# Kernel tuning notes

Measured on AMD Instinct MI355X. Metric: run time of the kernel, lower is better.

Reference implementation:

```python
import jax, jax.numpy as jnp
import numpy as np

D_MODEL = 512
D_STATE = 64
SEQ_LEN = 8192
BATCH = 8
LN_EPS = 1e-3  # keras LayerNormalization default epsilon
DELTA_MIN = 0.001
DELTA_MAX = 0.8 * (2.0 / D_STATE)  # default when use_hippo_init=True


def setup_inputs() -> dict:
    key = jax.random.key(0)
    ks = jax.random.split(key, 10)
    x = jax.random.normal(ks[0], (BATCH, SEQ_LEN, D_MODEL), dtype=jnp.float32)
    # Dense layers: glorot-uniform-ish init via scaled normal for simplicity
    def dense_w(k, fan_in, fan_out):
        lim = np.sqrt(6.0 / (fan_in + fan_out))
        return jax.random.uniform(k, (fan_in, fan_out), minval=-lim, maxval=lim, dtype=jnp.float32)
    W_in = dense_w(ks[1], D_MODEL, D_MODEL)
    b_in = jnp.zeros((D_MODEL,), jnp.float32)
    W_xs = dense_w(ks[2], D_MODEL, D_STATE)
    # HiPPO-LegS log init: A_log = log(n+1)
    A_log = jnp.log(jnp.arange(1, D_STATE + 1, dtype=jnp.float32))
    log_delta = jax.random.uniform(ks[3], (D_STATE,), minval=np.log(DELTA_MIN), maxval=np.log(DELTA_MAX), dtype=jnp.float32)
    B = jnp.ones((D_STATE,), jnp.float32)
    C = jax.random.normal(ks[4], (D_STATE,), dtype=jnp.float32)  # stddev=1.0
    D = jnp.ones((D_MODEL,), jnp.float32)
    W_so = dense_w(ks[5], D_STATE, D_MODEL)
    W_out = dense_w(ks[6], D_MODEL, D_MODEL)
    b_out = jnp.zeros((D_MODEL,), jnp.float32)
    ln_gamma = jnp.ones((D_MODEL,), jnp.float32)
    ln_beta = jnp.zeros((D_MODEL,), jnp.float32)
    return {
        "x": x, "ln_gamma": ln_gamma, "ln_beta": ln_beta,
        "W_in": W_in, "b_in": b_in, "W_xs": W_xs,
        "A_log": A_log, "log_delta": log_delta, "B": B, "C": C, "D": D,
        "W_so": W_so, "W_out": W_out, "b_out": b_out,
    }


def reference(x, ln_gamma, ln_beta, W_in, b_in, W_xs, A_log, log_delta, B, C, D, W_so, W_out, b_out):
    Bsz, L, dm = x.shape
    n_fft = 1 << int(np.ceil(np.log2(2 * L - 1)))
    residual = x
    # LayerNorm over last axis (keras default)
    mu = jnp.mean(x, axis=-1, keepdims=True)
    var = jnp.mean(jnp.square(x - mu), axis=-1, keepdims=True)
    xn = (x - mu) * jax.lax.rsqrt(var + LN_EPS) * ln_gamma + ln_beta
    z = xn @ W_in + b_in                       # (B, L, d_model)
    x_state = z @ W_xs                          # (B, L, d_state)
    # Diagonal SSM discretization (bilinear/Tustin)
    A = -jnp.exp(A_log)
    delta = jax.nn.softplus(log_delta)
    dA2 = delta * A / 2.0
    A_bar = (1.0 + dA2) / (1.0 - dA2)           # (d_state,)
    B_bar = delta / (1.0 - dA2) * B             # (d_state,)
    t = jnp.arange(L, dtype=jnp.float32)
    kernel = jnp.power(A_bar[None, :], t[:, None]) * B_bar[None, :]  # (L, d_state)
    # FFT convolution along time
    u_t = jnp.transpose(x_state, (0, 2, 1))     # (B, d_state, L)
    k_t = kernel.T                              # (d_state, L)
    u_f = jnp.fft.rfft(u_t, n=n_fft, axis=-1)
    k_f = jnp.fft.rfft(k_t, n=n_fft, axis=-1)
    y = jnp.fft.irfft(u_f * k_f[None, :, :], n=n_fft, axis=-1)[:, :, :L]
    y_state = jnp.transpose(y, (0, 2, 1))       # (B, L, d_state)
    y_state = y_state * C[None, None, :]
    y = y_state @ W_so                          # (B, L, d_model)
    y = y + D * z
    y = y @ W_out + b_out
    return y + residual
```

## Files before the change

### kernel.cpp

```cpp
#include <hip/hip_runtime.h>
#include <hip/hip_bf16.h>
#include <cstddef>
#include <cstdint>

#define DM 512
#define DS 64
#define L_SEQ 8192
#define NB 8
#define M_ROWS (NB * L_SEQ)
#define LN_EPS 1e-3f
#define NCHUNK 256
#define LCH 32

typedef __attribute__((ext_vector_type(8))) short short8;
typedef __attribute__((ext_vector_type(4))) float f32x4;
using bf16 = __hip_bfloat16;
using ushort_t = unsigned short;

__device__ __forceinline__ unsigned short f2bf(float f) {
    bf16 h = __float2bfloat16(f);
    return *reinterpret_cast<unsigned short*>(&h);
}

__device__ __forceinline__ int swzcol(int row, int col) {
    return (col & ~63) | (((((col >> 3) & 7) ^ (row & 7))) << 3) | (col & 7);
}

__device__ __forceinline__ size_t pkidx(int k, int n, int Kd32) {
    int n16 = n >> 4, fr = n & 15, kt = k >> 5, fq = (k >> 3) & 3, e = k & 7;
    return (((size_t)(n16 * Kd32 + kt) * 64 + fq * 16 + fr) << 3) + e;
}

__device__ __forceinline__ void gload_lds16(const void* g, void* l) {
    __builtin_amdgcn_global_load_lds(
        (const __attribute__((address_space(1))) void*)g,
        (__attribute__((address_space(3))) void*)l, 16, 0, 0);
}

template<int N> __device__ __forceinline__ void wait_vm() {
    static_assert(N == 0 || N == 2, "");
    if constexpr (N == 0) asm volatile("s_waitcnt vmcnt(0)" ::: "memory");
    else                  asm volatile("s_waitcnt vmcnt(2)" ::: "memory");
}

__device__ __forceinline__ void block_barrier() {
    asm volatile("" ::: "memory");
    __builtin_amdgcn_s_barrier();
    asm volatile("" ::: "memory");
}

__global__ __launch_bounds__(256) void prep(const float* __restrict__ W_so,
                                            const float* __restrict__ W_out,
                                            const float* __restrict__ W_in,
                                            const float* __restrict__ W_xs,
                                            const float* __restrict__ b_in,
                                            const float* __restrict__ b_out,
                                            const float* __restrict__ Dv,
                                            float* __restrict__ sWc2,
                                            float* __restrict__ sWc1,
                                            float* __restrict__ bc1,
                                            float* __restrict__ sWc3,
                                            float* __restrict__ bc2)
{
    int i = blockIdx.x * 256 + threadIdx.x;
    if (i < 32768) {
        int s = i >> 9, j = i & 511;
        float a = 0.f;
        for (int c = 0; c < 512; ++c) a += W_so[s * 512 + c] * W_out[c * 512 + j];
        sWc2[i] = a;
    } else if (i < 65536) {
        int idx = i - 32768; int k = idx >> 6, n = idx & 63;
        float a = 0.f;
        for (int c = 0; c < 512; ++c) a += W_in[k * 512 + c] * W_xs[c * 64 + n];
        sWc1[idx] = a;
    } else if (i < 65600) {
        int n = i - 65536;
        float a = 0.f;
        for (int c = 0; c < 512; ++c) a += b_in[c] * W_xs[c * 64 + n];
        bc1[n] = a;
    } else if (i < 327744) {
        int idx = i - 65600; int k = idx >> 9, j = idx & 511;
        float a = 0.f;
        for (int c = 0; c < 512; ++c) a += W_in[k * 512 + c] * Dv[c] * W_out[c * 512 + j];
        sWc3[idx] = a;
    } else if (i < 328256) {
        int j = i - 327744;
        float a = b_out[j];
        for (int c = 0; c < 512; ++c) a += b_in[c] * Dv[c] * W_out[c * 512 + j];
        bc2[j] = a;
    }
}

__global__ __launch_bounds__(256) void pack_all(const float* __restrict__ sWc3,
                                                const float* __restrict__ sWc1,
                                                const float* __restrict__ sWc2,
                                                ushort_t* __restrict__ Wc3Pk,
                                                ushort_t* __restrict__ Wc1Pk,
                                                ushort_t* __restrict__ Wc2Pk)
{
    int i = blockIdx.x * 256 + threadIdx.x;
    if (i < 262144) {
        int k = i >> 9, n = i & 511;
        Wc3Pk[pkidx(k, n, 16)] = f2bf(sWc3[i]);
    } else if (i < 294912) {
        int j = i - 262144; int k = j >> 6, n = j & 63;
        Wc1Pk[pkidx(k, n, 16)] = f2bf(sWc1[j]);
    } else if (i < 327680) {
        int j = i - 294912; int s = j >> 9, n = j & 511;
        Wc2Pk[pkidx(s, n, 2)] = f2bf(sWc2[j]);
    }
}

__global__ __launch_bounds__(64) void ln_kernel(const float* __restrict__ x,
                                                const float* __restrict__ gamma,
                                                const float* __restrict__ beta,
                                                ushort_t* __restrict__ xn)
{
    size_t row = blockIdx.x;
    int lane = threadIdx.x;
    const float4* xr = (const float4*)(x + row * DM);
    float4 v0 = xr[lane * 2];
    float4 v1 = xr[lane * 2 + 1];
    float s  = v0.x + v0.y + v0.z + v0.w + v1.x + v1.y + v1.z + v1.w;
    float s2 = v0.x*v0.x + v0.y*v0.y + v0.z*v0.z + v0.w*v0.w
             + v1.x*v1.x + v1.y*v1.y + v1.z*v1.z + v1.w*v1.w;
    #pragma unroll
    for (int off = 32; off > 0; off >>= 1) {
        s  += __shfl_xor(s,  off);
        s2 += __shfl_xor(s2, off);
    }
    float mu  = s * (1.0f / DM);
    float var = s2 * (1.0f / DM) - mu * mu;
    float rs  = rsqrtf(var + LN_EPS);
    const float4* g4 = (const float4*)gamma;
    const float4* b4 = (const float4*)beta;
    float4 g0 = g4[lane * 2], g1 = g4[lane * 2 + 1];
    float4 bb0 = b4[lane * 2], bb1 = b4[lane * 2 + 1];
    short8 o;
    o[0] = (short)f2bf((v0.x - mu) * rs * g0.x + bb0.x);
    o[1] = (short)f2bf((v0.y - mu) * rs * g0.y + bb0.y);
    o[2] = (short)f2bf((v0.z - mu) * rs * g0.z + bb0.z);
    o[3] = (short)f2bf((v0.w - mu) * rs * g0.w + bb0.w);
    o[4] = (short)f2bf((v1.x - mu) * rs * g1.x + bb1.x);
    o[5] = (short)f2bf((v1.y - mu) * rs * g1.y + bb1.y);
    o[6] = (short)f2bf((v1.z - mu) * rs * g1.z + bb1.z);
    o[7] = (short)f2bf((v1.w - mu) * rs * g1.w + bb1.w);
    int g = (lane & 7) ^ ((int)row & 7);
    *(short8*)(xn + row * DM + (lane >> 3) * 64 + g * 8) = o;
}

__device__ __forceinline__ void store_out(float* C, size_t i, float v) { C[i] = v; }
__device__ __forceinline__ void store_out(bf16* C, size_t i, float v)  { C[i] = __float2bfloat16(v); }

template<int BN, int WR, int WC, typename OutT, bool DUAL, bool HB, bool HA, bool SWZO>
__global__ __launch_bounds__(512, 4) void gemm_bp(const ushort_t* __restrict__ A1,
                                                  const ushort_t* __restrict__ B1,
                                                  const ushort_t* __restrict__ A2,
                                                  const ushort_t* __restrict__ B2,
                                                  const float* __restrict__ bias,
                                                  const float* __restrict__ aux,
                                                  OutT* __restrict__ C,
                                                  int M, int N, int K2)
{
    constexpr int BM = 128;
    constexpr int MF = BM / (16 * WR), NF = BN / (16 * WC);
    static_assert(NF == 2, "b ping-pong arrays assume NF==2");
    __shared__ unsigned char LDS[3][BM * 128];

    const int tid = threadIdx.x;
    const int lane = tid & 63, w = tid >> 6;
    const int fr = lane & 15, fq = lane >> 4;
    const int wr = w % WR, wc = w / WR;

    const int ny = N / BN;
    const int per = (int)gridDim.x >> 3;
    const int lg = ((int)blockIdx.x & 7) * per + ((int)blockIdx.x >> 3);
    const size_t bm0 = (size_t)(lg / ny) * BM;
    const int bn0 = (lg % ny) * BN;
    const int nk = (DUAL ? 1 : 0) + K2 / 64;

    f32x4 acc[MF][NF];
    #pragma unroll
    for (int m = 0; m < MF; ++m)
        #pragma unroll
        for (int n = 0; n < NF; ++n)
            acc[m][n] = (f32x4){0.f, 0.f, 0.f, 0.f};

    auto stage = [&](int buf, int t) {
        #pragma unroll
        for (int j = 0; j < 2; ++j) {
            int r = j * 64 + (tid >> 3);
            const ushort_t* src;
            if constexpr (DUAL) {
                if (t == 0) src = A1 + (bm0 + r) * (size_t)64 + (tid & 7) * 8;
                else        src = A2 + (bm0 + r) * (size_t)512 + (size_t)(t - 1) * 64 + (tid & 7) * 8;
            } else {
                src = A2 + (bm0 + r) * (size_t)K2 + (size_t)t * 64 + (tid & 7) * 8;
            }
            gload_lds16(src, &LDS[buf][j * 8192 + w * 1024]);
        }
    };

    auto loadB = [&](short8 (&bb)[2][2], int t) {
        #pragma unroll
        for (int h = 0; h < 2; ++h)
            #pragma unroll
            for (int n = 0; n < NF; ++n) {
                int n16g = (bn0 + wc * (BN / WC) + n * 16) >> 4;
                const ushort_t* p;
                if constexpr (DUAL) {
                    if (t == 0) p = B1 + (((size_t)(n16g * 2 + h) * 64 + lane) << 3);
                    else        p = B2 + (((size_t)(n16g * 16 + (t - 1) * 2 + h) * 64 + lane) << 3);
                } else {
                    p = B2 + (((size_t)(n16g * (K2 / 32) + t * 2 + h) * 64 + lane) << 3);
                }
                bb[h][n] = *(const short8*)p;
            }
    };

    auto compute = [&](int buf, const short8 (&bb)[2][2]) {
        #pragma unroll
        for (int h = 0; h < 2; ++h) {
            short8 af[MF];
            #pragma unroll
            for (int m = 0; m < MF; ++m) {
                int row = wr * (BM / WR) + m * 16 + fr;
                int g = (h * 4 + fq) ^ (row & 7);
                af[m] = *(const short8*)&LDS[buf][row * 128 + g * 16];
            }
            #pragma unroll
            for (int m = 0; m < MF; ++m)
                #pragma unroll
                for (int n = 0; n < NF; ++n)
                    acc[m][n] = __builtin_amdgcn_mfma_f32_16x16x32_bf16(af[m], bb[h][n], acc[m][n], 0, 0, 0);
        }
    };

    short8 bX[2][2], bY[2][2];
    stage(0, 0);
    loadB(bX, 0);
    if (nk > 1) stage(1, 1);

    #define PHASE(T, BCUR, BNEXT)                                            \
        do {                                                                 \
            if ((T) + 1 < nk) wait_vm<2>(); else wait_vm<0>();               \
            block_barrier();                                                 \
            if ((T) + 1 < nk) loadB(BNEXT, (T) + 1);                         \
            if ((T) + 2 < nk) stage(((T) + 2) % 3, (T) + 2);                 \
            __builtin_amdgcn_sched_barrier(0);                               \
            compute((T) % 3, BCUR);                                          \
        } while (0)

    for (int t = 0; t < nk; t += 2) {
        PHASE(t, bX, bY);
        if (t + 1 < nk) PHASE(t + 1, bY, bX);
    }
    #undef PHASE

    #pragma unroll
    for (int n = 0; n < NF; ++n) {
        int coll = wc * (BN / WC) + n * 16 + fr;
        int colg = bn0 + coll;
        float bv = HB ? bias[colg] : 0.f;
        #pragma unroll
        for (int m = 0; m < MF; ++m) {
            int rowl = wr * (BM / WR) + m * 16 + fq * 4;
            #pragma unroll
            for (int r = 0; r < 4; ++r) {
                size_t row = bm0 + rowl + r;
                float v = acc[m][n][r] + bv;
                if constexpr (HA) v += aux[row * (size_t)N + colg];
                size_t oc = SWZO ? (size_t)swzcol(rowl + r, colg) : (size_t)colg;
                store_out(C, row * (size_t)N + oc, v);
            }
        }
    }
}

__device__ __forceinline__ void ssm_params(const float* A_log, const float* log_delta,
                                           const float* Bv, int n, float& Ab, float& Bb)
{
    float A  = -expf(A_log[n]);
    float dl = log1pf(expf(log_delta[n]));
    float dA2 = dl * A * 0.5f;
    float inv = 1.0f / (1.0f - dA2);
    Ab = (1.0f + dA2) * inv;
    Bb = dl * inv * Bv[n];
}

__global__ __launch_bounds__(64) void scan_pass1(const float* __restrict__ xs,
                                                 const float* __restrict__ A_log,
                                                 const float* __restrict__ log_delta,
                                                 const float* __restrict__ Bv,
                                                 float* __restrict__ carry)
{
    int b = blockIdx.x / NCHUNK;
    int c = blockIdx.x % NCHUNK;
    int n = threadIdx.x;
    float Ab, Bb;
    ssm_params(A_log, log_delta, Bv, n, Ab, Bb);
    size_t base = ((size_t)b * L_SEQ + (size_t)c * LCH) * DS + n;
    float h = 0.0f;
    for (int t = 0; t < LCH; ++t)
        h = Ab * h + Bb * xs[base + (size_t)t * DS];
    carry[((size_t)b * NCHUNK + c) * DS + n] = h;
}

__global__ __launch_bounds__(64) void scan_pass2(const float* __restrict__ A_log,
                                                 const float* __restrict__ log_delta,
                                                 const float* __restrict__ Bv,
                                                 const float* __restrict__ carry,
                                                 float* __restrict__ hin)
{
    int b = blockIdx.x;
    int n = threadIdx.x;
    float Ab, Bb;
    ssm_params(A_log, log_delta, Bv, n, Ab, Bb);
    float powA = powf(Ab, (float)LCH);
    float h = 0.0f;
    for (int c = 0; c < NCHUNK; ++c) {
        size_t idx = ((size_t)b * NCHUNK + c) * DS + n;
        hin[idx] = h;
        h = powA * h + carry[idx];
    }
}

__global__ __launch_bounds__(64) void scan_pass3(const float* __restrict__ xs,
                                                 const float* __restrict__ A_log,
                                                 const float* __restrict__ log_delta,
                                                 const float* __restrict__ Bv,
                                                 const float* __restrict__ Cv,
                                                 const float* __restrict__ hin,
                                                 ushort_t* __restrict__ ys)
{
    int b = blockIdx.x / NCHUNK;
    int c = blockIdx.x % NCHUNK;
    int n = threadIdx.x;
    float Ab, Bb;
    ssm_params(A_log, log_delta, Bv, n, Ab, Bb);
    float Cn = Cv[n];
    size_t base = ((size_t)b * L_SEQ + (size_t)c * LCH) * DS + n;
    size_t rowbase = ((size_t)b * L_SEQ + (size_t)c * LCH) * DS;
    float h = hin[((size_t)b * NCHUNK + c) * DS + n];
    for (int t = 0; t < LCH; ++t) {
        h = Ab * h + Bb * xs[base + (size_t)t * DS];
        int col = (((n >> 3) ^ (t & 7)) << 3) | (n & 7);
        ys[rowbase + (size_t)t * DS + col] = f2bf(Cn * h);
    }
}

extern "C" void kernel_launch(void* const* d_in, const int* in_sizes, int n_in,
                              void* d_out, int out_size, void* d_ws, size_t ws_size,
                              hipStream_t stream)
{
    const float* x         = (const float*)d_in[0];
    const float* ln_gamma  = (const float*)d_in[1];
    const float* ln_beta   = (const float*)d_in[2];
    const float* W_in      = (const float*)d_in[3];
    const float* b_in      = (const float*)d_in[4];
    const float* W_xs      = (const float*)d_in[5];
    const float* A_log     = (const float*)d_in[6];
    const float* log_delta = (const float*)d_in[7];
    const float* Bv        = (const float*)d_in[8];
    const float* Cv        = (const float*)d_in[9];
    const float* Dv        = (const float*)d_in[10];
    const float* W_so      = (const float*)d_in[11];
    const float* W_out     = (const float*)d_in[12];
    const float* b_out     = (const float*)d_in[13];
    float* out = (float*)d_out;

    const size_t M = M_ROWS;
    float*    xs_f   = (float*)d_ws;
    ushort_t* xn_b   = (ushort_t*)(xs_f + M * DS);
    ushort_t* ys_b   = xn_b + M * (size_t)DM;
    ushort_t* Wc3Pk  = ys_b + M * (size_t)DS;
    ushort_t* Wc1Pk  = Wc3Pk + (size_t)DM * DM;
    ushort_t* Wc2Pk  = Wc1Pk + (size_t)DM * DS;
    float*    sWc2   = (float*)(Wc2Pk + (size_t)DS * DM);
    float*    sWc1   = sWc2 + (size_t)DS * DM;
    float*    bc1    = sWc1 + (size_t)DM * DS;
    float*    sWc3   = bc1 + 64;
    float*    bc2    = sWc3 + (size_t)DM * DM;
    float*    carry  = bc2 + DM;
    float*    hin    = carry + NB * NCHUNK * DS;

    prep<<<dim3(1283), dim3(256), 0, stream>>>(W_so, W_out, W_in, W_xs, b_in, b_out, Dv,
                                               sWc2, sWc1, bc1, sWc3, bc2);
    pack_all<<<dim3(1280), dim3(256), 0, stream>>>(sWc3, sWc1, sWc2, Wc3Pk, Wc1Pk, Wc2Pk);
    ln_kernel<<<dim3((unsigned)M), dim3(64), 0, stream>>>(x, ln_gamma, ln_beta, xn_b);
    gemm_bp<64, 4, 2, float, false, true, false, false>
        <<<dim3(M / 128), dim3(512), 0, stream>>>(nullptr, nullptr, xn_b, Wc1Pk,
                                                  bc1, nullptr, xs_f, (int)M, DS, DM);
    scan_pass1<<<dim3(NB * NCHUNK), dim3(64), 0, stream>>>(xs_f, A_log, log_delta, Bv, carry);
    scan_pass2<<<dim3(NB), dim3(64), 0, stream>>>(A_log, log_delta, Bv, carry, hin);
    scan_pass3<<<dim3(NB * NCHUNK), dim3(64), 0, stream>>>(xs_f, A_log, log_delta, Bv, Cv, hin, ys_b);
    gemm_bp<256, 1, 8, float, true, true, true, false>
        <<<dim3((M / 128) * (DM / 256)), dim3(512), 0, stream>>>(ys_b, Wc2Pk, xn_b, Wc3Pk,
                                                                 bc2, x, out, (int)M, DM, DM);
}
```

Measured before the change: 235.7 us.

## Make output GEMM persistent over multiple M tiles with overlapped epilogue and aux prefetch

The GEMM kernel now processes MT consecutive 128-row tiles per block, flattening tiles and K-steps into one pipelined stage sequence. The next tile's A loads stay in flight while the current tile's epilogue runs, and residual (aux) values are prefetched into registers before the last K-step of each tile. The final GEMM also moves from BN=256 (1x8 warps) to BN=128 (2x4 warps) with four M tiles per block, which cuts block count and launch/prologue overhead. The costs are more registers held for paux and hand-tuned vmcnt wait counts that must exactly match the number of outstanding loads.

```diff
diff --git a/kernel.cpp b/kernel.cpp
--- a/kernel.cpp
+++ b/kernel.cpp
@@ -38,9 +38,11 @@
 }
 
 template<int N> __device__ __forceinline__ void wait_vm() {
-    static_assert(N == 0 || N == 2, "");
-    if constexpr (N == 0) asm volatile("s_waitcnt vmcnt(0)" ::: "memory");
-    else                  asm volatile("s_waitcnt vmcnt(2)" ::: "memory");
+    static_assert(N == 0 || N == 2 || N == 18 || N == 34, "");
+    if constexpr (N == 0)       asm volatile("s_waitcnt vmcnt(0)" ::: "memory");
+    else if constexpr (N == 2)  asm volatile("s_waitcnt vmcnt(2)" ::: "memory");
+    else if constexpr (N == 18) asm volatile("s_waitcnt vmcnt(18)" ::: "memory");
+    else                        asm volatile("s_waitcnt vmcnt(34)" ::: "memory");
 }
 
 __device__ __forceinline__ void block_barrier() {
@@ -152,7 +154,8 @@
 __device__ __forceinline__ void store_out(float* C, size_t i, float v) { C[i] = v; }
 __device__ __forceinline__ void store_out(bf16* C, size_t i, float v)  { C[i] = __float2bfloat16(v); }
 
-template<int BN, int WR, int WC, typename OutT, bool DUAL, bool HB, bool HA, bool SWZO>
+template<int BN, int WR, int WC, int MT, int NKT, typename OutT,
+         bool DUAL, bool HB, bool HA, bool SWZO>
 __global__ __launch_bounds__(512, 4) void gemm_bp(const ushort_t* __restrict__ A1,
                                                   const ushort_t* __restrict__ B1,
                                                   const ushort_t* __restrict__ A2,
@@ -160,10 +163,12 @@
                                                   const float* __restrict__ bias,
                                                   const float* __restrict__ aux,
                                                   OutT* __restrict__ C,
-                                                  int M, int N, int K2)
+                                                  int M, int N)
 {
     constexpr int BM = 128;
     constexpr int MF = BM / (16 * WR), NF = BN / (16 * WC);
+    constexpr int NS = MT * NKT;
+    constexpr int WEPI = 2 + MF * NF * 4;
     static_assert(NF == 2, "b ping-pong arrays assume NF==2");
     __shared__ unsigned char LDS[3][BM * 128];
 
@@ -175,9 +180,8 @@
     const int ny = N / BN;
     const int per = (int)gridDim.x >> 3;
     const int lg = ((int)blockIdx.x & 7) * per + ((int)blockIdx.x >> 3);
-    const size_t bm0 = (size_t)(lg / ny) * BM;
+    const size_t bm0 = (size_t)(lg / ny) * (BM * MT);
     const int bn0 = (lg % ny) * BN;
-    const int nk = (DUAL ? 1 : 0) + K2 / 64;
 
     f32x4 acc[MF][NF];
     #pragma unroll
@@ -186,22 +190,27 @@
         for (int n = 0; n < NF; ++n)
             acc[m][n] = (f32x4){0.f, 0.f, 0.f, 0.f};
 
-    auto stage = [&](int buf, int t) {
+    float paux[MF][NF][4];
+
+    auto stage = [&](int buf, int s) {
+        int tt = s / NKT, kk = s % NKT;
+        size_t rb = bm0 + (size_t)tt * BM;
         #pragma unroll
         for (int j = 0; j < 2; ++j) {
             int r = j * 64 + (tid >> 3);
             const ushort_t* src;
             if constexpr (DUAL) {
-                if (t == 0) src = A1 + (bm0 + r) * (size_t)64 + (tid & 7) * 8;
-                else        src = A2 + (bm0 + r) * (size_t)512 + (size_t)(t - 1) * 64 + (tid & 7) * 8;
+                if (kk == 0) src = A1 + (rb + r) * (size_t)64 + (tid & 7) * 8;
+                else         src = A2 + (rb + r) * (size_t)512 + (size_t)(kk - 1) * 64 + (tid & 7) * 8;
             } else {
-                src = A2 + (bm0 + r) * (size_t)K2 + (size_t)t * 64 + (tid & 7) * 8;
+                src = A2 + (rb + r) * (size_t)512 + (size_t)kk * 64 + (tid & 7) * 8;
             }
             gload_lds16(src, &LDS[buf][j * 8192 + w * 1024]);
         }
     };
 
-    auto loadB = [&](short8 (&bb)[2][2], int t) {
+    auto loadB = [&](short8 (&bb)[2][2], int s) {
+        int kk = s % NKT;
         #pragma unroll
         for (int h = 0; h < 2; ++h)
             #pragma unroll
@@ -209,10 +218,10 @@
                 int n16g = (bn0 + wc * (BN / WC) + n * 16) >> 4;
                 const ushort_t* p;
                 if constexpr (DUAL) {
-                    if (t == 0) p = B1 + (((size_t)(n16g * 2 + h) * 64 + lane) << 3);
-                    else        p = B2 + (((size_t)(n16g * 16 + (t - 1) * 2 + h) * 64 + lane) << 3);
+                    if (kk == 0) p = B1 + (((size_t)(n16g * 2 + h) * 64 + lane) << 3);
+                    else         p = B2 + (((size_t)(n16g * 16 + (kk - 1) * 2 + h) * 64 + lane) << 3);
                 } else {
-                    p = B2 + (((size_t)(n16g * (K2 / 32) + t * 2 + h) * 64 + lane) << 3);
+                    p = B2 + (((size_t)(n16g * 16 + kk * 2 + h) * 64 + lane) << 3);
                 }
                 bb[h][n] = *(const short8*)p;
             }
@@ -236,45 +245,70 @@
         }
     };
 
+    auto prefetch_aux = [&](int tt) {
+        if constexpr (HA) {
+            #pragma unroll
+            for (int n = 0; n < NF; ++n) {
+                int colg = bn0 + wc * (BN / WC) + n * 16 + fr;
+                #pragma unroll
+                for (int m = 0; m < MF; ++m) {
+                    int rowl = wr * (BM / WR) + m * 16 + fq * 4;
+                    #pragma unroll
+                    for (int r = 0; r < 4; ++r)
+                        paux[m][n][r] = aux[(bm0 + (size_t)tt * BM + rowl + r) * (size_t)N + colg];
+                }
+            }
+        }
+    };
+
+    auto epilogue = [&](int tt) {
+        #pragma unroll
+        for (int n = 0; n < NF; ++n) {
+            int coll = wc * (BN / WC) + n * 16 + fr;
+            int colg = bn0 + coll;
+            float bv = HB ? bias[colg] : 0.f;
+            #pragma unroll
+            for (int m = 0; m < MF; ++m) {
+                int rowl = wr * (BM / WR) + m * 16 + fq * 4;
+                #pragma unroll
+                for (int r = 0; r < 4; ++r) {
+                    size_t row = bm0 + (size_t)tt * BM + rowl + r;
+                    float v = acc[m][n][r] + bv;
+                    if constexpr (HA) v += paux[m][n][r];
+                    size_t oc = SWZO ? (size_t)swzcol(rowl + r, colg) : (size_t)colg;
+                    store_out(C, row * (size_t)N + oc, v);
+                    acc[m][n][r] = 0.f;
+                }
+            }
+        }
+    };
+
     short8 bX[2][2], bY[2][2];
     stage(0, 0);
     loadB(bX, 0);
-    if (nk > 1) stage(1, 1);
-
-    #define PHASE(T, BCUR, BNEXT)                                            \
+    if (NS > 1) stage(1, 1);
+
+    #define PHASE(S, BCUR, BNEXT)                                            \
         do {                                                                 \
-            if ((T) + 1 < nk) wait_vm<2>(); else wait_vm<0>();               \
+            int tt_ = (S) / NKT, kk_ = (S) % NKT;                            \
+            if ((S) == NS - 1)           wait_vm<0>();                       \
+            else if (kk_ == 0 && (S))    wait_vm<WEPI>();                    \
+            else                         wait_vm<2>();                       \
             block_barrier();                                                 \
-            if ((T) + 1 < nk) loadB(BNEXT, (T) + 1);                         \
-            if ((T) + 2 < nk) stage(((T) + 2) % 3, (T) + 2);                 \
+            bool tl_ = (kk_ == NKT - 1);                                     \
+            if (HA && tl_) prefetch_aux(tt_);                                \
+            if ((S) + 1 < NS) loadB(BNEXT, (S) + 1);                         \
+            if ((S) + 2 < NS) stage(((S) + 2) % 3, (S) + 2);                 \
             __builtin_amdgcn_sched_barrier(0);                               \
-            compute((T) % 3, BCUR);                                          \
+            compute((S) % 3, BCUR);                                          \
+            if (tl_) epilogue(tt_);                                          \
         } while (0)
 
-    for (int t = 0; t < nk; t += 2) {
-        PHASE(t, bX, bY);
-        if (t + 1 < nk) PHASE(t + 1, bY, bX);
+    for (int s = 0; s < NS; s += 2) {
+        PHASE(s, bX, bY);
+        if (s + 1 < NS) PHASE(s + 1, bY, bX);
     }
     #undef PHASE
-
-    #pragma unroll
-    for (int n = 0; n < NF; ++n) {
-        int coll = wc * (BN / WC) + n * 16 + fr;
-        int colg = bn0 + coll;
-        float bv = HB ? bias[colg] : 0.f;
-        #pragma unroll
-        for (int m = 0; m < MF; ++m) {
-            int rowl = wr * (BM / WR) + m * 16 + fq * 4;
-            #pragma unroll
-            for (int r = 0; r < 4; ++r) {
-                size_t row = bm0 + rowl + r;
-                float v = acc[m][n][r] + bv;
-                if constexpr (HA) v += aux[row * (size_t)N + colg];
-                size_t oc = SWZO ? (size_t)swzcol(rowl + r, colg) : (size_t)colg;
-                store_out(C, row * (size_t)N + oc, v);
-            }
-        }
-    }
 }
 
 __device__ __forceinline__ void ssm_params(const float* A_log, const float* log_delta,
@@ -388,13 +422,13 @@
                                                sWc2, sWc1, bc1, sWc3, bc2);
     pack_all<<<dim3(1280), dim3(256), 0, stream>>>(sWc3, sWc1, sWc2, Wc3Pk, Wc1Pk, Wc2Pk);
     ln_kernel<<<dim3((unsigned)M), dim3(64), 0, stream>>>(x, ln_gamma, ln_beta, xn_b);
-    gemm_bp<64, 4, 2, float, false, true, false, false>
+    gemm_bp<64, 4, 2, 1, 8, float, false, true, false, false>
         <<<dim3(M / 128), dim3(512), 0, stream>>>(nullptr, nullptr, xn_b, Wc1Pk,
-                                                  bc1, nullptr, xs_f, (int)M, DS, DM);
+                                                  bc1, nullptr, xs_f, (int)M, DS);
     scan_pass1<<<dim3(NB * NCHUNK), dim3(64), 0, stream>>>(xs_f, A_log, log_delta, Bv, carry);
     scan_pass2<<<dim3(NB), dim3(64), 0, stream>>>(A_log, log_delta, Bv, carry, hin);
     scan_pass3<<<dim3(NB * NCHUNK), dim3(64), 0, stream>>>(xs_f, A_log, log_delta, Bv, Cv, hin, ys_b);
-    gemm_bp<256, 1, 8, float, true, true, true, false>
-        <<<dim3((M / 128) * (DM / 256)), dim3(512), 0, stream>>>(ys_b, Wc2Pk, xn_b, Wc3Pk,
-                                                                 bc2, x, out, (int)M, DM, DM);
-}
+    gemm_bp<128, 2, 4, 4, 9, float, true, true, true, false>
+        <<<dim3((M / 512) * (DM / 128)), dim3(512), 0, stream>>>(ys_b, Wc2Pk, xn_b, Wc3Pk,
+                                                                 bc2, x, out, (int)M, DM);
+}
```

Measured after the change: 305.9 us. 1.3x slower.
